# Kernel tuning notes

Hardware: AMD Instinct MI355X
Metric: run time of the kernel (lower is better)

## Reference

```python
import jax, jax.numpy as jnp
import numpy as np

B, C, T = 32, 256, 4096


def _depthwise(x, w, pad):
    # x: [B, C, T], w: [C, 1, k] (torch grouped-conv layout), groups = C
    return jax.lax.conv_general_dilated(
        x, w, window_strides=(1,), padding=[(pad, pad)],
        dimension_numbers=("NCH", "OIH", "NCH"), feature_group_count=x.shape[1])


def setup_inputs() -> dict:
    key = jax.random.key(0)
    ks = jax.random.split(key, 9)
    def u(k, shape, fan_in):
        s = 1.0 / np.sqrt(fan_in)
        return jax.random.uniform(k, shape, jnp.float32, -s, s)
    return {
        "x": jax.random.normal(ks[0], (B, C, T), jnp.float32),
        "w1": u(ks[1], (C, C, 1), C),      # 1x1 conv, full depth
        "b1": u(ks[2], (C,), C),
        "w3": u(ks[3], (C, 1, 3), 3),      # 1x3 depthwise (groups=C)
        "b3": u(ks[4], (C,), 3),
        "w5": u(ks[5], (C, 1, 5), 5),      # 1x5 depthwise (groups=C)
        "b5": u(ks[6], (C,), 5),
        "wc": u(ks[7], (C, 3, 1), 3),      # combine: Conv1d(3C, C, 1, groups=C)
        "bc": u(ks[8], (C,), 3),
    }


def reference(x, w1, b1, w3, b3, w5, b5, wc, bc):
    a = jax.nn.gelu(x, approximate=False)  # torch GELU default is exact erf
    # 1x1 conv over all channels == per-timestep GEMM
    out1 = jnp.einsum("bct,oc->bot", a, w1[:, :, 0]) + b1[None, :, None]
    out3 = _depthwise(a, w3, 1) + b3[None, :, None]
    out5 = _depthwise(a, w5, 2) + b5[None, :, None]
    # per-channel interleave: [c0_1, c0_3, c0_5, c1_1, ...] -> [B, C, 3, T]
    inter = jnp.stack((out1, out3, out5), axis=2)
    # grouped 1x1 combine conv (groups=C): each output channel mixes its 3 branch outputs
    out = jnp.einsum("bcjt,cj->bct", inter, wc[:, :, 0]) + bc[None, :, None]
    return out + x
```

## Files before the change

### kernel.cpp

```cpp
#include <hip/hip_runtime.h>
#include <stdint.h>

#define BATCH 32
#define CH    256
#define TLEN  4096
#define TN    32
#define NRW   36
#define TPAD  4100
#define SST   36

typedef short    bf16x8 __attribute__((ext_vector_type(8)));
typedef float    f32x4  __attribute__((ext_vector_type(4)));
typedef uint16_t u16x4  __attribute__((ext_vector_type(4)));
typedef uint16_t u16x8  __attribute__((ext_vector_type(8)));

__device__ __attribute__((aligned(16))) uint16_t g_wpk[CH * CH];
__device__ __attribute__((aligned(16))) float g_tap[5 * CH];
__device__ __attribute__((aligned(16))) float g_bias[CH];

static __device__ __forceinline__ uint16_t f32_to_bf16(float f) {
    uint32_t u = __builtin_bit_cast(uint32_t, f);
    u += 0x7FFFu + ((u >> 16) & 1u);
    return (uint16_t)(u >> 16);
}
static __device__ __forceinline__ float bf16_to_f32(uint16_t h) {
    uint32_t u = ((uint32_t)h) << 16;
    return __builtin_bit_cast(float, u);
}
static __device__ __forceinline__ float gelu_fast(float x) {
    const float A = 2.3022082f;
    const float B = 0.10294331f;
    float x2 = x * x;
    float z  = x * fmaf(x2, B, A);
    float e  = exp2f(z);
    float r  = __builtin_amdgcn_rcpf(1.0f + e);
    return fmaf(-x, r, x);
}

__global__ void prep_kernel(const float* __restrict__ w1, const float* __restrict__ b1,
                            const float* __restrict__ w3, const float* __restrict__ b3,
                            const float* __restrict__ w5, const float* __restrict__ b5,
                            const float* __restrict__ wc, const float* __restrict__ bc) {
    const int o = blockIdx.x;
    const int c = threadIdx.x;
    const float wc0 = wc[o * 3 + 0];
    const int s = c >> 5, g = (c >> 3) & 3, e = c & 7;
    g_wpk[(s * CH + o) * 32 + g * 8 + e] = f32_to_bf16(wc0 * w1[o * CH + c]);
    if (c == 0) {
        const float wc1 = wc[o * 3 + 1], wc2 = wc[o * 3 + 2];
        g_tap[0 * CH + o] = wc2 * w5[o * 5 + 0];
        g_tap[1 * CH + o] = wc1 * w3[o * 3 + 0] + wc2 * w5[o * 5 + 1];
        g_tap[2 * CH + o] = wc1 * w3[o * 3 + 1] + wc2 * w5[o * 5 + 2];
        g_tap[3 * CH + o] = wc1 * w3[o * 3 + 2] + wc2 * w5[o * 5 + 3];
        g_tap[4 * CH + o] = wc2 * w5[o * 5 + 4];
        g_bias[o] = wc0 * b1[o] + wc1 * b3[o] + wc2 * b5[o] + bc[o];
    }
}

__global__ __launch_bounds__(256, 4)
void gelu_tr_kernel(const float* __restrict__ x, uint16_t* __restrict__ aT) {
    __shared__ __attribute__((aligned(16))) uint16_t sL[64 * 72];

    const int tid = threadIdx.x;
    const int tb = blockIdx.x, cb = blockIdx.y, b = blockIdx.z;
    const int t0 = tb * 64, c0 = cb * 64;

    {
        const int cr = tid >> 2;
        const int q  = tid & 3;
        const float* xr = x + ((size_t)(b * CH + c0 + cr)) * TLEN + t0 + q * 16;
        f32x4 v0 = *(const f32x4*)(xr + 0);
        f32x4 v1 = *(const f32x4*)(xr + 4);
        f32x4 v2 = *(const f32x4*)(xr + 8);
        f32x4 v3 = *(const f32x4*)(xr + 12);
        u16x8 p0, p1;
#pragma unroll
        for (int j = 0; j < 4; ++j) {
            p0[j]     = f32_to_bf16(gelu_fast(v0[j]));
            p0[4 + j] = f32_to_bf16(gelu_fast(v1[j]));
            p1[j]     = f32_to_bf16(gelu_fast(v2[j]));
            p1[4 + j] = f32_to_bf16(gelu_fast(v3[j]));
        }
        const int b0 = (((q * 2 + 0) ^ (cr >> 3)) << 3);
        const int b1 = (((q * 2 + 1) ^ (cr >> 3)) << 3);
        *(u16x8*)(&sL[cr * 72 + b0]) = p0;
        *(u16x8*)(&sL[cr * 72 + b1]) = p1;
    }
    __syncthreads();

    uint16_t* aTb = aT + (size_t)b * TPAD * CH;
#pragma unroll
    for (int i = 0; i < 2; ++i) {
        const int idx = tid + i * 256;
        const int tr  = idx >> 3;
        const int ch  = idx & 7;
        const int t   = t0 + tr;
        const int swz = (t & 7) << 3;
        const int cin = (tr & 7) | ((((tr >> 3) ^ ch) & 7) << 3);
        u16x8 o;
#pragma unroll
        for (int j = 0; j < 8; ++j) o[j] = sL[(ch * 8 + j) * 72 + cin];
        *(u16x8*)(&aTb[(size_t)(2 + t) * CH + ((c0 + ch * 8) ^ swz)]) = o;
    }
    if (tb == 0) {
        const int pr = tid >> 6;
        const int cc = c0 + (tid & 63);
        const int prow = (pr < 2) ? pr : (4098 + (pr - 2));
        const int tmod = (pr < 2) ? (6 + pr) : (pr - 2);
        aTb[(size_t)prow * CH + (cc ^ (tmod << 3))] = 0;
    }
}

__global__ __launch_bounds__(512, 2)
void gemm_kernel(const uint16_t* __restrict__ aT, const float* __restrict__ x,
                 float* __restrict__ out) {
    __shared__ __attribute__((aligned(16))) uint16_t sA[NRW * CH];

    const int tid  = threadIdx.x;
    const int lane = tid & 63;
    const int wid  = tid >> 6;
    const int b    = blockIdx.y;
    const int t0   = blockIdx.x * TN;

    const float* __restrict__ xb = x + (size_t)b * CH * TLEN;
    float* __restrict__ ob = out + (size_t)b * CH * TLEN;

    const int m0   = wid * 32;
    const int colt = lane & 15;
    const int kgrp = (lane >> 4) * 8;

    bf16x8 wfr[8][2];
#pragma unroll
    for (int s = 0; s < 8; ++s)
#pragma unroll
        for (int mi = 0; mi < 2; ++mi) {
            const int co = m0 + mi * 16 + colt;
            wfr[s][mi] = *(const bf16x8*)(g_wpk + (s * CH + co) * 32 + kgrp);
        }

    {
        const u16x8* gsrc = (const u16x8*)(aT + (size_t)b * TPAD * CH + (size_t)t0 * CH);
        u16x8 stg[2], stgT;
#pragma unroll
        for (int i = 0; i < 2; ++i) stg[i] = gsrc[tid + i * 512];
        const bool tail = (tid < 128);
        if (tail) stgT = gsrc[tid + 1024];
        u16x8* ldst = (u16x8*)sA;
#pragma unroll
        for (int i = 0; i < 2; ++i) ldst[tid + i * 512] = stg[i];
        if (tail) ldst[tid + 1024] = stgT;
    }
    __syncthreads();

    f32x4 acc[2][2];
    const f32x4 vzero = {0.f, 0.f, 0.f, 0.f};
#pragma unroll
    for (int mi = 0; mi < 2; ++mi)
#pragma unroll
        for (int ni = 0; ni < 2; ++ni) acc[mi][ni] = vzero;

    const int swzB = (colt & 7) << 3;
    int rowB[2];
#pragma unroll
    for (int ni = 0; ni < 2; ++ni) rowB[ni] = (ni * 16 + colt + 2) * CH;

    bf16x8 bfb[2][2];
#pragma unroll
    for (int ni = 0; ni < 2; ++ni)
        bfb[0][ni] = *(const bf16x8*)(&sA[rowB[ni] + (kgrp ^ swzB)]);
#pragma unroll
    for (int s = 0; s < 8; ++s) {
        const int cur = s & 1, nxt = cur ^ 1;
        if (s < 7) {
            const int cin = (s + 1) * 32 + kgrp;
#pragma unroll
            for (int ni = 0; ni < 2; ++ni)
                bfb[nxt][ni] = *(const bf16x8*)(&sA[rowB[ni] + (cin ^ swzB)]);
        }
#pragma unroll
        for (int mi = 0; mi < 2; ++mi)
#pragma unroll
            for (int ni = 0; ni < 2; ++ni)
                acc[mi][ni] = __builtin_amdgcn_mfma_f32_16x16x32_bf16(wfr[s][mi], bfb[cur][ni], acc[mi][ni], 0, 0, 0);
    }

    const int rg = (lane >> 4) * 4;
    int swzA[5];
#pragma unroll
    for (int k = 0; k < 5; ++k) swzA[k] = ((colt + k + 6) & 7) << 3;
#pragma unroll
    for (int mi = 0; mi < 2; ++mi) {
        const int c = m0 + mi * 16 + rg;
        const f32x4 tp0 = *(const f32x4*)(g_tap + 0 * CH + c);
        const f32x4 tp1 = *(const f32x4*)(g_tap + 1 * CH + c);
        const f32x4 tp2 = *(const f32x4*)(g_tap + 2 * CH + c);
        const f32x4 tp3 = *(const f32x4*)(g_tap + 3 * CH + c);
        const f32x4 tp4 = *(const f32x4*)(g_tap + 4 * CH + c);
        const f32x4 bsv = *(const f32x4*)(g_bias + c);
#pragma unroll
        for (int ni = 0; ni < 2; ++ni) {
            const int t = ni * 16 + colt;
            u16x4 a0 = *(const u16x4*)(&sA[(t + 0) * CH + (c ^ swzA[0])]);
            u16x4 a1 = *(const u16x4*)(&sA[(t + 1) * CH + (c ^ swzA[1])]);
            u16x4 a2 = *(const u16x4*)(&sA[(t + 2) * CH + (c ^ swzA[2])]);
            u16x4 a3 = *(const u16x4*)(&sA[(t + 3) * CH + (c ^ swzA[3])]);
            u16x4 a4 = *(const u16x4*)(&sA[(t + 4) * CH + (c ^ swzA[4])]);
#pragma unroll
            for (int r = 0; r < 4; ++r) {
                float d = tp0[r] * bf16_to_f32(a0[r]);
                d = fmaf(tp1[r], bf16_to_f32(a1[r]), d);
                d = fmaf(tp2[r], bf16_to_f32(a2[r]), d);
                d = fmaf(tp3[r], bf16_to_f32(a3[r]), d);
                d = fmaf(tp4[r], bf16_to_f32(a4[r]), d);
                acc[mi][ni][r] += d + bsv[r];
            }
        }
    }
    __syncthreads();

    float* __restrict__ sw = ((float*)sA) + wid * (16 * SST);
    const int ci = lane >> 2;
    const int q  = lane & 3;

#pragma unroll
    for (int mi = 0; mi < 2; ++mi) {
        const int cc = m0 + mi * 16 + ci;
        const float* xrow = xb + (size_t)cc * TLEN + t0 + q * 8;
        f32x4 xv0 = *(const f32x4*)(xrow + 0);
        f32x4 xv1 = *(const f32x4*)(xrow + 4);
#pragma unroll
        for (int ni = 0; ni < 2; ++ni) {
            const int t = ni * 16 + colt;
#pragma unroll
            for (int r = 0; r < 4; ++r) sw[(rg + r) * SST + t] = acc[mi][ni][r];
        }
        float* orow = ob + (size_t)cc * TLEN + t0 + q * 8;
        const float* srow = sw + ci * SST + q * 8;
        f32x4 s0 = *(const f32x4*)(srow + 0);
        f32x4 s1 = *(const f32x4*)(srow + 4);
        *(f32x4*)(orow + 0) = s0 + xv0;
        *(f32x4*)(orow + 4) = s1 + xv1;
    }
}

extern "C" void kernel_launch(void* const* d_in, const int* in_sizes, int n_in,
                              void* d_out, int out_size, void* d_ws, size_t ws_size,
                              hipStream_t stream) {
    const float* x  = (const float*)d_in[0];
    const float* w1 = (const float*)d_in[1];
    const float* b1 = (const float*)d_in[2];
    const float* w3 = (const float*)d_in[3];
    const float* b3 = (const float*)d_in[4];
    const float* w5 = (const float*)d_in[5];
    const float* b5 = (const float*)d_in[6];
    const float* wc = (const float*)d_in[7];
    const float* bc = (const float*)d_in[8];
    float* out = (float*)d_out;
    uint16_t* aT = (uint16_t*)d_ws;

    prep_kernel<<<dim3(CH), dim3(CH), 0, stream>>>(w1, b1, w3, b3, w5, b5, wc, bc);
    gelu_tr_kernel<<<dim3(TLEN / 64, CH / 64, BATCH), dim3(256), 0, stream>>>(x, aT);
    gemm_kernel<<<dim3(TLEN / TN, BATCH), dim3(512), 0, stream>>>(aT, x, out);
}
```

Baseline: 116.6 us.

## Make GEMM blocks persistent over 8 time tiles with double-buffered prefetch

Each gemm block now walks 8 consecutive 32-step time tiles instead of one. The weight fragments are loaded into registers once per block rather than once per tile. The next tile's activations are prefetched into registers while the current tile computes, then stored into a second LDS buffer. This targets repeated weight loads and exposed global-load latency, but the grid shrinks to 512 blocks, which may underfill the GPU, and it adds LDS use and a loop-carried barrier.

```diff
diff --git a/kernel.cpp b/kernel.cpp
--- a/kernel.cpp
+++ b/kernel.cpp
@@ -5,6 +5,7 @@
 #define CH    256
 #define TLEN  4096
 #define TN    32
+#define NT    8
 #define NRW   36
 #define TPAD  4100
 #define SST   36
@@ -114,20 +115,25 @@
 __global__ __launch_bounds__(512, 2)
 void gemm_kernel(const uint16_t* __restrict__ aT, const float* __restrict__ x,
                  float* __restrict__ out) {
-    __shared__ __attribute__((aligned(16))) uint16_t sA[NRW * CH];
+    __shared__ __attribute__((aligned(16))) uint16_t sA[2][NRW * CH];
 
     const int tid  = threadIdx.x;
     const int lane = tid & 63;
     const int wid  = tid >> 6;
     const int b    = blockIdx.y;
-    const int t0   = blockIdx.x * TN;
+    const int t0b  = blockIdx.x * (TN * NT);
 
     const float* __restrict__ xb = x + (size_t)b * CH * TLEN;
     float* __restrict__ ob = out + (size_t)b * CH * TLEN;
+    const u16x8* __restrict__ gB = (const u16x8*)(aT + (size_t)b * TPAD * CH);
 
     const int m0   = wid * 32;
     const int colt = lane & 15;
     const int kgrp = (lane >> 4) * 8;
+    const int rg   = (lane >> 4) * 4;
+    const int ci   = lane >> 2;
+    const int q4   = lane & 3;
+    const bool tail = (tid < 128);
 
     bf16x8 wfr[8][2];
 #pragma unroll
@@ -139,107 +145,128 @@
         }
 
     {
-        const u16x8* gsrc = (const u16x8*)(aT + (size_t)b * TPAD * CH + (size_t)t0 * CH);
-        u16x8 stg[2], stgT;
-#pragma unroll
-        for (int i = 0; i < 2; ++i) stg[i] = gsrc[tid + i * 512];
-        const bool tail = (tid < 128);
-        if (tail) stgT = gsrc[tid + 1024];
-        u16x8* ldst = (u16x8*)sA;
-#pragma unroll
-        for (int i = 0; i < 2; ++i) ldst[tid + i * 512] = stg[i];
-        if (tail) ldst[tid + 1024] = stgT;
+        const u16x8* g0 = gB + (size_t)t0b * 32;
+        u16x8 s0_ = g0[tid];
+        u16x8 s1_ = g0[tid + 512];
+        u16x8 sT_;
+        if (tail) sT_ = g0[tid + 1024];
+        u16x8* d = (u16x8*)sA[0];
+        d[tid] = s0_; d[tid + 512] = s1_;
+        if (tail) d[tid + 1024] = sT_;
     }
     __syncthreads();
-
-    f32x4 acc[2][2];
-    const f32x4 vzero = {0.f, 0.f, 0.f, 0.f};
-#pragma unroll
-    for (int mi = 0; mi < 2; ++mi)
-#pragma unroll
-        for (int ni = 0; ni < 2; ++ni) acc[mi][ni] = vzero;
 
     const int swzB = (colt & 7) << 3;
     int rowB[2];
 #pragma unroll
     for (int ni = 0; ni < 2; ++ni) rowB[ni] = (ni * 16 + colt + 2) * CH;
-
-    bf16x8 bfb[2][2];
-#pragma unroll
-    for (int ni = 0; ni < 2; ++ni)
-        bfb[0][ni] = *(const bf16x8*)(&sA[rowB[ni] + (kgrp ^ swzB)]);
-#pragma unroll
-    for (int s = 0; s < 8; ++s) {
-        const int cur = s & 1, nxt = cur ^ 1;
-        if (s < 7) {
-            const int cin = (s + 1) * 32 + kgrp;
-#pragma unroll
-            for (int ni = 0; ni < 2; ++ni)
-                bfb[nxt][ni] = *(const bf16x8*)(&sA[rowB[ni] + (cin ^ swzB)]);
-        }
+    int swzA[5];
+#pragma unroll
+    for (int k = 0; k < 5; ++k) swzA[k] = ((colt + k + 6) & 7) << 3;
+
+    for (int i = 0; i < NT; ++i) {
+        const int cur = i & 1, nxt = cur ^ 1;
+        const int t0 = t0b + i * TN;
+
+        u16x8 p0, p1, pT;
+        if (i + 1 < NT) {
+            const u16x8* gn = gB + (size_t)(t0 + TN) * 32;
+            p0 = gn[tid];
+            p1 = gn[tid + 512];
+            if (tail) pT = gn[tid + 1024];
+        }
+        f32x4 xv[2][2];
+#pragma unroll
+        for (int mi = 0; mi < 2; ++mi) {
+            const int cc = m0 + mi * 16 + ci;
+            const float* xr = xb + (size_t)cc * TLEN + t0 + q4 * 8;
+            xv[mi][0] = *(const f32x4*)(xr + 0);
+            xv[mi][1] = *(const f32x4*)(xr + 4);
+        }
+
+        const uint16_t* __restrict__ sAc = sA[cur];
+
+        f32x4 acc[2][2];
+        const f32x4 vzero = {0.f, 0.f, 0.f, 0.f};
 #pragma unroll
         for (int mi = 0; mi < 2; ++mi)
 #pragma unroll
-            for (int ni = 0; ni < 2; ++ni)
-                acc[mi][ni] = __builtin_amdgcn_mfma_f32_16x16x32_bf16(wfr[s][mi], bfb[cur][ni], acc[mi][ni], 0, 0, 0);
-    }
-
-    const int rg = (lane >> 4) * 4;
-    int swzA[5];
-#pragma unroll
-    for (int k = 0; k < 5; ++k) swzA[k] = ((colt + k + 6) & 7) << 3;
-#pragma unroll
-    for (int mi = 0; mi < 2; ++mi) {
-        const int c = m0 + mi * 16 + rg;
-        const f32x4 tp0 = *(const f32x4*)(g_tap + 0 * CH + c);
-        const f32x4 tp1 = *(const f32x4*)(g_tap + 1 * CH + c);
-        const f32x4 tp2 = *(const f32x4*)(g_tap + 2 * CH + c);
-        const f32x4 tp3 = *(const f32x4*)(g_tap + 3 * CH + c);
-        const f32x4 tp4 = *(const f32x4*)(g_tap + 4 * CH + c);
-        const f32x4 bsv = *(const f32x4*)(g_bias + c);
-#pragma unroll
-        for (int ni = 0; ni < 2; ++ni) {
-            const int t = ni * 16 + colt;
-            u16x4 a0 = *(const u16x4*)(&sA[(t + 0) * CH + (c ^ swzA[0])]);
-            u16x4 a1 = *(const u16x4*)(&sA[(t + 1) * CH + (c ^ swzA[1])]);
-            u16x4 a2 = *(const u16x4*)(&sA[(t + 2) * CH + (c ^ swzA[2])]);
-            u16x4 a3 = *(const u16x4*)(&sA[(t + 3) * CH + (c ^ swzA[3])]);
-            u16x4 a4 = *(const u16x4*)(&sA[(t + 4) * CH + (c ^ swzA[4])]);
-#pragma unroll
-            for (int r = 0; r < 4; ++r) {
-                float d = tp0[r] * bf16_to_f32(a0[r]);
-                d = fmaf(tp1[r], bf16_to_f32(a1[r]), d);
-                d = fmaf(tp2[r], bf16_to_f32(a2[r]), d);
-                d = fmaf(tp3[r], bf16_to_f32(a3[r]), d);
-                d = fmaf(tp4[r], bf16_to_f32(a4[r]), d);
-                acc[mi][ni][r] += d + bsv[r];
+            for (int ni = 0; ni < 2; ++ni) acc[mi][ni] = vzero;
+
+        bf16x8 bfb[2][2];
+#pragma unroll
+        for (int ni = 0; ni < 2; ++ni)
+            bfb[0][ni] = *(const bf16x8*)(&sAc[rowB[ni] + (kgrp ^ swzB)]);
+#pragma unroll
+        for (int s = 0; s < 8; ++s) {
+            const int c2 = s & 1, nx = c2 ^ 1;
+            if (s < 7) {
+                const int cin = (s + 1) * 32 + kgrp;
+#pragma unroll
+                for (int ni = 0; ni < 2; ++ni)
+                    bfb[nx][ni] = *(const bf16x8*)(&sAc[rowB[ni] + (cin ^ swzB)]);
             }
-        }
-    }
-    __syncthreads();
-
-    float* __restrict__ sw = ((float*)sA) + wid * (16 * SST);
-    const int ci = lane >> 2;
-    const int q  = lane & 3;
-
-#pragma unroll
-    for (int mi = 0; mi < 2; ++mi) {
-        const int cc = m0 + mi * 16 + ci;
-        const float* xrow = xb + (size_t)cc * TLEN + t0 + q * 8;
-        f32x4 xv0 = *(const f32x4*)(xrow + 0);
-        f32x4 xv1 = *(const f32x4*)(xrow + 4);
-#pragma unroll
-        for (int ni = 0; ni < 2; ++ni) {
-            const int t = ni * 16 + colt;
-#pragma unroll
-            for (int r = 0; r < 4; ++r) sw[(rg + r) * SST + t] = acc[mi][ni][r];
-        }
-        float* orow = ob + (size_t)cc * TLEN + t0 + q * 8;
-        const float* srow = sw + ci * SST + q * 8;
-        f32x4 s0 = *(const f32x4*)(srow + 0);
-        f32x4 s1 = *(const f32x4*)(srow + 4);
-        *(f32x4*)(orow + 0) = s0 + xv0;
-        *(f32x4*)(orow + 4) = s1 + xv1;
+#pragma unroll
+            for (int mi = 0; mi < 2; ++mi)
+#pragma unroll
+                for (int ni = 0; ni < 2; ++ni)
+                    acc[mi][ni] = __builtin_amdgcn_mfma_f32_16x16x32_bf16(wfr[s][mi], bfb[c2][ni], acc[mi][ni], 0, 0, 0);
+        }
+
+#pragma unroll
+        for (int mi = 0; mi < 2; ++mi) {
+            const int c = m0 + mi * 16 + rg;
+            const f32x4 tp0 = *(const f32x4*)(g_tap + 0 * CH + c);
+            const f32x4 tp1 = *(const f32x4*)(g_tap + 1 * CH + c);
+            const f32x4 tp2 = *(const f32x4*)(g_tap + 2 * CH + c);
+            const f32x4 tp3 = *(const f32x4*)(g_tap + 3 * CH + c);
+            const f32x4 tp4 = *(const f32x4*)(g_tap + 4 * CH + c);
+            const f32x4 bsv = *(const f32x4*)(g_bias + c);
+#pragma unroll
+            for (int ni = 0; ni < 2; ++ni) {
+                const int t = ni * 16 + colt;
+                u16x4 a0 = *(const u16x4*)(&sAc[(t + 0) * CH + (c ^ swzA[0])]);
+                u16x4 a1 = *(const u16x4*)(&sAc[(t + 1) * CH + (c ^ swzA[1])]);
+                u16x4 a2 = *(const u16x4*)(&sAc[(t + 2) * CH + (c ^ swzA[2])]);
+                u16x4 a3 = *(const u16x4*)(&sAc[(t + 3) * CH + (c ^ swzA[3])]);
+                u16x4 a4 = *(const u16x4*)(&sAc[(t + 4) * CH + (c ^ swzA[4])]);
+#pragma unroll
+                for (int r = 0; r < 4; ++r) {
+                    float d = tp0[r] * bf16_to_f32(a0[r]);
+                    d = fmaf(tp1[r], bf16_to_f32(a1[r]), d);
+                    d = fmaf(tp2[r], bf16_to_f32(a2[r]), d);
+                    d = fmaf(tp3[r], bf16_to_f32(a3[r]), d);
+                    d = fmaf(tp4[r], bf16_to_f32(a4[r]), d);
+                    acc[mi][ni][r] += d + bsv[r];
+                }
+            }
+        }
+        __syncthreads();
+
+        float* __restrict__ sw = ((float*)sA[cur]) + wid * (16 * SST);
+#pragma unroll
+        for (int mi = 0; mi < 2; ++mi) {
+#pragma unroll
+            for (int ni = 0; ni < 2; ++ni) {
+                const int t = ni * 16 + colt;
+#pragma unroll
+                for (int r = 0; r < 4; ++r) sw[(rg + r) * SST + t] = acc[mi][ni][r];
+            }
+            const int cc = m0 + mi * 16 + ci;
+            float* orow = ob + (size_t)cc * TLEN + t0 + q4 * 8;
+            const float* srow = sw + ci * SST + q4 * 8;
+            f32x4 s0 = *(const f32x4*)(srow + 0);
+            f32x4 s1 = *(const f32x4*)(srow + 4);
+            *(f32x4*)(orow + 0) = s0 + xv[mi][0];
+            *(f32x4*)(orow + 4) = s1 + xv[mi][1];
+        }
+
+        if (i + 1 < NT) {
+            u16x8* d = (u16x8*)sA[nxt];
+            d[tid] = p0; d[tid + 512] = p1;
+            if (tail) d[tid + 1024] = pT;
+        }
+        __syncthreads();
     }
 }
 
@@ -260,5 +287,5 @@
 
     prep_kernel<<<dim3(CH), dim3(CH), 0, stream>>>(w1, b1, w3, b3, w5, b5, wc, bc);
     gelu_tr_kernel<<<dim3(TLEN / 64, CH / 64, BATCH), dim3(256), 0, stream>>>(x, aT);
-    gemm_kernel<<<dim3(TLEN / TN, BATCH), dim3(512), 0, stream>>>(aT, x, out);
-}
+    gemm_kernel<<<dim3(TLEN / (TN * NT), BATCH), dim3(512), 0, stream>>>(aT, x, out);
+}
```

After: 104.5 us. 10.4% less time.
